# Kernel optimization log

Measured on AMD Instinct MI355X. Metric: run time of the kernel, lower is better.

Reference implementation:

```python
import jax, jax.numpy as jnp
import numpy as np

H = 32       # num_attention_heads
KV = 8       # num_key_value_heads
D = 128      # head_dim
HID = 4096   # hidden_size
EPS = 1e-6   # rms_norm_eps
BASE = 1000000.0  # rope_theta


def setup_inputs() -> dict:
    key = jax.random.key(0)
    ks = jax.random.split(key, 5)
    B, S = 1, 2048
    s = 0.02
    return {
        "x": jax.random.normal(ks[0], (B, S, HID), jnp.float32),
        "wq": jax.random.normal(ks[1], (H * D, HID), jnp.float32) * s,
        "wk": jax.random.normal(ks[2], (KV * D, HID), jnp.float32) * s,
        "wv": jax.random.normal(ks[3], (KV * D, HID), jnp.float32) * s,
        "wo": jax.random.normal(ks[4], (HID, H * D), jnp.float32) * s,
        "q_norm_w": jnp.ones((D,), jnp.float32),
        "k_norm_w": jnp.ones((D,), jnp.float32),
    }


def _rms(x, w):
    # F.rms_norm over last dim (head_dim), computed in fp32 then cast back
    x32 = x.astype(jnp.float32)
    y = x32 * jax.lax.rsqrt(jnp.mean(x32 * x32, axis=-1, keepdims=True) + EPS)
    return (y * w.astype(jnp.float32)).astype(x.dtype)


def _rope_tables(S, dtype):
    pair = jnp.arange(0, D, 2, dtype=jnp.float32)
    theta = 1.0 / (BASE ** (pair / D))                       # [D/2]
    ang = jnp.arange(S, dtype=jnp.float32)[:, None] * theta  # [S, D/2]
    ang = jnp.concatenate([ang, ang], axis=-1)               # [S, D]
    return jnp.cos(ang).astype(dtype), jnp.sin(ang).astype(dtype)


def _rope(x, cos, sin):
    # x: [B, H, S, D]; rotate_half convention (cat of two halves)
    half = D // 2
    rot = jnp.concatenate([-x[..., half:], x[..., :half]], axis=-1)
    return x * cos + rot * sin


def reference(x, wq, wk, wv, wo, q_norm_w, k_norm_w):
    B, S, _ = x.shape
    q = (x @ wq.T).reshape(B, S, H, D)
    k = (x @ wk.T).reshape(B, S, KV, D)
    v = (x @ wv.T).reshape(B, S, KV, D)
    q = _rms(q, q_norm_w).transpose(0, 2, 1, 3)   # [B, H, S, D]
    k = _rms(k, k_norm_w).transpose(0, 2, 1, 3)   # [B, KV, S, D]
    v = v.transpose(0, 2, 1, 3)                   # [B, KV, S, D]
    cos, sin = _rope_tables(S, x.dtype)
    q = _rope(q, cos, sin)
    k = _rope(k, cos, sin)
    # GQA: group Q heads over KV heads, causal SDPA
    G = H // KV
    qg = q.reshape(B, KV, G, S, D)
    scale = 1.0 / np.sqrt(D).astype(np.float32)
    scores = jnp.einsum('bkgsd,bktd->bkgst', qg, k) * scale  # [B,KV,G,S,S]
    causal = jnp.tril(jnp.ones((S, S), dtype=bool))
    scores = jnp.where(causal, scores, jnp.asarray(-jnp.inf, scores.dtype))
    p = jax.nn.softmax(scores, axis=-1)
    out = jnp.einsum('bkgst,bktd->bkgsd', p, v)               # [B,KV,G,S,D]
    out = out.reshape(B, H, S, D).transpose(0, 2, 1, 3).reshape(B, S, H * D)
    return out @ wo.T
```

## Files before the change

kernel.cpp:

```cpp
#include <hip/hip_runtime.h>
#include <hip/hip_bf16.h>

#define S_LEN   2048
#define HID_SZ  4096
#define NH      32
#define NKV     8
#define HD      128
#define EPS_F   1e-6f
#define SM_SCALE 0.08838834764831845f

typedef __attribute__((ext_vector_type(8))) short bf16x8;
typedef __attribute__((ext_vector_type(4))) float f32x4;

#define AS1(p) ((__attribute__((address_space(1))) void*)(p))
#define AS3(p) ((__attribute__((address_space(3))) void*)(p))

__device__ __forceinline__ short f2b(float f) {
  unsigned u = __builtin_bit_cast(unsigned, f);
  unsigned r = (u + 0x7fffu + ((u >> 16) & 1u)) >> 16;
  return (short)(unsigned short)r;
}

__global__ __launch_bounds__(256) void cvt_f32_bf16(const float* __restrict__ in,
                                                    short* __restrict__ out, int n4) {
  int i = blockIdx.x * 256 + threadIdx.x;
  if (i >= n4) return;
  float4 f = reinterpret_cast<const float4*>(in)[i];
  short4 o;
  o.x = f2b(f.x); o.y = f2b(f.y); o.z = f2b(f.z); o.w = f2b(f.w);
  reinterpret_cast<short4*>(out)[i] = o;
}

__global__ void rope_tables_k(float* __restrict__ cosT, float* __restrict__ sinT) {
  int s = blockIdx.x;
  int j = threadIdx.x;
  float theta = exp2f(-(float)(2 * j) * (19.931568569324174f / 128.0f));
  float ang = (float)s * theta;
  float sv, cv;
  sincosf(ang, &sv, &cv);
  cosT[s * 64 + j] = cv;
  sinT[s * 64 + j] = sv;
}

__global__ __launch_bounds__(256)
void rmsrope_k(const float* __restrict__ src, int srcStride, int srcCol,
               const float* __restrict__ w,
               const float* __restrict__ cosT, const float* __restrict__ sinT,
               short* __restrict__ dst, int heads) {
  int gw   = blockIdx.x * 4 + (threadIdx.x >> 6);
  int lane = threadIdx.x & 63;
  int s = gw / heads;
  int h = gw - s * heads;
  const float* p = src + (size_t)s * srcStride + srcCol + h * HD;
  float x0 = p[lane], x1 = p[lane + 64];
  float ss = x0 * x0 + x1 * x1;
#pragma unroll
  for (int off = 1; off < 64; off <<= 1) ss += __shfl_xor(ss, off);
  float r = rsqrtf(ss * (1.0f / 128.0f) + EPS_F);
  float y0 = x0 * r * w[lane];
  float y1 = x1 * r * w[lane + 64];
  float c = cosT[s * 64 + lane], sn = sinT[s * 64 + lane];
  float o0 = y0 * c - y1 * sn;
  float o1 = y1 * c + y0 * sn;
  short* d = dst + ((size_t)h * S_LEN + s) * HD;
  d[lane]      = f2b(o0);
  d[lane + 64] = f2b(o1);
}

__global__ __launch_bounds__(256)
void vtrans_k(const float* __restrict__ qkv, short* __restrict__ vt) {
  __shared__ float t[64][65];
  int s0 = blockIdx.x * 64;
  int d0 = blockIdx.y * 64;
  int kv = blockIdx.z;
  int j  = threadIdx.x & 63;
  int i0 = threadIdx.x >> 6;
#pragma unroll
  for (int r = 0; r < 16; ++r) {
    int i = i0 * 16 + r;
    t[i][j] = qkv[(size_t)(s0 + i) * 6144 + 5120 + kv * HD + d0 + j];
  }
  __syncthreads();
#pragma unroll
  for (int r = 0; r < 16; ++r) {
    int i = i0 * 16 + r;
    vt[((size_t)kv * HD + d0 + i) * S_LEN + s0 + j] = f2b(t[j][i]);
  }
}

__global__ __launch_bounds__(256)
void gemm_bt_k(const short* __restrict__ A, const short* __restrict__ B,
               float* __restrict__ C, int M, int N, int K) {
  __shared__ short As[128 * 32];
  __shared__ short Bs[128 * 32];
  int tid  = threadIdx.x;
  int lane = tid & 63;
  int wave = tid >> 6;
  int wr = wave >> 1, wc = wave & 1;
  int m0 = blockIdx.y * 128, n0 = blockIdx.x * 128;
  f32x4 acc[4][4] = {};
  int row16 = lane & 15;
  int kg    = (lane >> 4) << 3;
  int c0 = tid, c1 = tid + 256;
  const size_t rA0 = (size_t)(m0 + (c0 >> 2)) * K + ((c0 & 3) << 3);
  const size_t rA1 = (size_t)(m0 + (c1 >> 2)) * K + ((c1 & 3) << 3);
  const size_t rB0 = (size_t)(n0 + (c0 >> 2)) * K + ((c0 & 3) << 3);
  const size_t rB1 = (size_t)(n0 + (c1 >> 2)) * K + ((c1 & 3) << 3);
  for (int kt = 0; kt < K; kt += 32) {
    __builtin_amdgcn_global_load_lds(AS1(A + rA0 + kt), AS3(&As[c0 * 8]), 16, 0, 0);
    __builtin_amdgcn_global_load_lds(AS1(A + rA1 + kt), AS3(&As[c1 * 8]), 16, 0, 0);
    __builtin_amdgcn_global_load_lds(AS1(B + rB0 + kt), AS3(&Bs[c0 * 8]), 16, 0, 0);
    __builtin_amdgcn_global_load_lds(AS1(B + rB1 + kt), AS3(&Bs[c1 * 8]), 16, 0, 0);
    __syncthreads();
    bf16x8 af[4], bf[4];
#pragma unroll
    for (int i = 0; i < 4; ++i)
      af[i] = *reinterpret_cast<const bf16x8*>(&As[(wr * 64 + i * 16 + row16) * 32 + kg]);
#pragma unroll
    for (int j = 0; j < 4; ++j)
      bf[j] = *reinterpret_cast<const bf16x8*>(&Bs[(wc * 64 + j * 16 + row16) * 32 + kg]);
#pragma unroll
    for (int i = 0; i < 4; ++i)
#pragma unroll
      for (int j = 0; j < 4; ++j)
        acc[i][j] = __builtin_amdgcn_mfma_f32_16x16x32_bf16(af[i], bf[j], acc[i][j], 0, 0, 0);
    __syncthreads();
  }
  int rsub = (lane >> 4) << 2;
#pragma unroll
  for (int i = 0; i < 4; ++i)
#pragma unroll
    for (int j = 0; j < 4; ++j) {
      size_t base = (size_t)(m0 + wr * 64 + i * 16 + rsub) * N + (n0 + wc * 64 + j * 16 + row16);
#pragma unroll
      for (int reg = 0; reg < 4; ++reg)
        C[base + (size_t)reg * N] = acc[i][j][reg];
    }
}

__global__ __launch_bounds__(256)
void attn_k(const short* __restrict__ Qr, const short* __restrict__ Kr,
            const short* __restrict__ Vt, short* __restrict__ Ob) {
  constexpr int PP = 72;
  __shared__ short Kl[64 * 128];
  __shared__ short Vl[128 * 64];
  __shared__ short Pl[4][16 * PP];
  int qb = (int)gridDim.x - 1 - (int)blockIdx.x;
  int h  = blockIdx.y;
  int kvh = h >> 2;
  int tid = threadIdx.x, wave = tid >> 6, lane = tid & 63;
  int row16 = lane & 15, kg = (lane >> 4) << 3, rsub = (lane >> 4) << 2;
  int colb  = (lane >> 4) << 4;
  int swz   = (row16 & 7) << 4;
  int qrow0 = qb * 64 + wave * 16;

  bf16x8 qf[4];
  {
    const short* qp = Qr + ((size_t)h * S_LEN + qrow0 + row16) * HD + kg;
#pragma unroll
    for (int ks = 0; ks < 4; ++ks)
      qf[ks] = *reinterpret_cast<const bf16x8*>(qp + ks * 32);
  }
  f32x4 o[8] = {};
  float mrow[4], lrow[4];
#pragma unroll
  for (int r = 0; r < 4; ++r) { mrow[r] = -3.0e38f; lrow[r] = 0.0f; }

  const short* Kb = Kr + (size_t)kvh * S_LEN * HD;
  const short* Vb = Vt + (size_t)kvh * HD * S_LEN;

  for (int kt = 0; kt <= qb; ++kt) {
    const short* Kt = Kb + (size_t)kt * 64 * HD;
#pragma unroll
    for (int r = 0; r < 4; ++r) {
      int c = tid + r * 256;
      int krow = c >> 4, ch = c & 15;
      int sch = (ch & 8) | ((ch ^ krow) & 7);
      __builtin_amdgcn_global_load_lds(AS1(Kt + krow * HD + sch * 8),
                                       AS3(&Kl[c * 8]), 16, 0, 0);
    }
#pragma unroll
    for (int r = 0; r < 4; ++r) {
      int c = tid + r * 256;
      int dr = c >> 3, ch = c & 7;
      int sch = (ch ^ dr) & 7;
      __builtin_amdgcn_global_load_lds(AS1(Vb + (size_t)dr * S_LEN + kt * 64 + sch * 8),
                                       AS3(&Vl[c * 8]), 16, 0, 0);
    }
    __syncthreads();

    f32x4 s4[4];
#pragma unroll
    for (int nc = 0; nc < 4; ++nc) {
      int R = nc * 16 + row16;
      const char* rowp = (const char*)Kl + R * 256;
      f32x4 a = {};
#pragma unroll
      for (int ks = 0; ks < 4; ++ks) {
        bf16x8 kf = *reinterpret_cast<const bf16x8*>(rowp + ((ks * 64 + colb) ^ swz));
        a = __builtin_amdgcn_mfma_f32_16x16x32_bf16(qf[ks], kf, a, 0, 0, 0);
      }
      s4[nc] = a;
    }

    bool diag = (kt == qb);
    float mt[4] = {-3.0e38f, -3.0e38f, -3.0e38f, -3.0e38f};
#pragma unroll
    for (int nc = 0; nc < 4; ++nc)
#pragma unroll
      for (int reg = 0; reg < 4; ++reg) {
        float v = s4[nc][reg] * SM_SCALE;
        if (diag && (kt * 64 + nc * 16 + row16) > (qrow0 + rsub + reg)) v = -3.0e38f;
        s4[nc][reg] = v;
        mt[reg] = fmaxf(mt[reg], v);
      }
#pragma unroll
    for (int reg = 0; reg < 4; ++reg)
#pragma unroll
      for (int off = 1; off < 16; off <<= 1)
        mt[reg] = fmaxf(mt[reg], __shfl_xor(mt[reg], off));

    float sc[4], st[4];
#pragma unroll
    for (int reg = 0; reg < 4; ++reg) {
      float mnew = fmaxf(mrow[reg], mt[reg]);
      sc[reg] = __expf(mrow[reg] - mnew);
      mrow[reg] = mnew;
      st[reg] = 0.0f;
    }
#pragma unroll
    for (int nc = 0; nc < 4; ++nc)
#pragma unroll
      for (int reg = 0; reg < 4; ++reg) {
        float p = __expf(s4[nc][reg] - mrow[reg]);
        s4[nc][reg] = p;
        st[reg] += p;
      }
#pragma unroll
    for (int reg = 0; reg < 4; ++reg) {
#pragma unroll
      for (int off = 1; off < 16; off <<= 1)
        st[reg] += __shfl_xor(st[reg], off);
      lrow[reg] = lrow[reg] * sc[reg] + st[reg];
    }
#pragma unroll
    for (int i = 0; i < 8; ++i) {
      f32x4 t = o[i];
      t[0] *= sc[0]; t[1] *= sc[1]; t[2] *= sc[2]; t[3] *= sc[3];
      o[i] = t;
    }

#pragma unroll
    for (int nc = 0; nc < 4; ++nc)
#pragma unroll
      for (int reg = 0; reg < 4; ++reg)
        Pl[wave][(rsub + reg) * PP + nc * 16 + row16] = f2b(s4[nc][reg]);

#pragma unroll
    for (int ks = 0; ks < 2; ++ks) {
      bf16x8 pf = *reinterpret_cast<const bf16x8*>(&Pl[wave][row16 * PP + ks * 32 + kg]);
#pragma unroll
      for (int nc = 0; nc < 8; ++nc) {
        int R = nc * 16 + row16;
        const char* rowp = (const char*)Vl + R * 128;
        bf16x8 vf = *reinterpret_cast<const bf16x8*>(rowp + ((ks * 64 + colb) ^ swz));
        o[nc] = __builtin_amdgcn_mfma_f32_16x16x32_bf16(pf, vf, o[nc], 0, 0, 0);
      }
    }
    __syncthreads();
  }

#pragma unroll
  for (int nc = 0; nc < 8; ++nc)
#pragma unroll
    for (int reg = 0; reg < 4; ++reg) {
      float val = o[nc][reg] * (1.0f / lrow[reg]);
      int srow = qrow0 + rsub + reg;
      Ob[(size_t)srow * HID_SZ + h * HD + nc * 16 + row16] = f2b(val);
    }
}

extern "C" void kernel_launch(void* const* d_in, const int* in_sizes, int n_in,
                              void* d_out, int out_size, void* d_ws, size_t ws_size,
                              hipStream_t stream) {
  const float* x   = (const float*)d_in[0];
  const float* wq  = (const float*)d_in[1];
  const float* wk  = (const float*)d_in[2];
  const float* wv  = (const float*)d_in[3];
  const float* wo  = (const float*)d_in[4];
  const float* qnw = (const float*)d_in[5];
  const float* knw = (const float*)d_in[6];
  float* out = (float*)d_out;

  char* ws = (char*)d_ws;
  short* xb    = (short*)(ws);
  short* attnb = (short*)(ws);
  short* wqkvb = (short*)(ws + (16ull  << 20));
  short* wob   = (short*)(ws + (16ull  << 20));
  float* qkvf  = (float*)(ws + (64ull  << 20));
  short* qr    = (short*)(ws + (112ull << 20));
  short* kr    = (short*)(ws + (128ull << 20));
  short* vt    = (short*)(ws + (132ull << 20));
  float* cosT  = (float*)(ws + (136ull << 20));
  float* sinT  = (float*)(ws + (136ull << 20) + (512ull << 10));

  cvt_f32_bf16<<<8192,  256, 0, stream>>>(x,  xb,    2097152);
  cvt_f32_bf16<<<16384, 256, 0, stream>>>(wq, wqkvb,                       4194304);
  cvt_f32_bf16<<<4096,  256, 0, stream>>>(wk, wqkvb + (size_t)4096 * 4096, 1048576);
  cvt_f32_bf16<<<4096,  256, 0, stream>>>(wv, wqkvb + (size_t)5120 * 4096, 1048576);

  rope_tables_k<<<2048, 64, 0, stream>>>(cosT, sinT);

  gemm_bt_k<<<dim3(48, 16), 256, 0, stream>>>(xb, wqkvb, qkvf, 2048, 6144, 4096);

  cvt_f32_bf16<<<16384, 256, 0, stream>>>(wo, wob, 4194304);

  rmsrope_k<<<16384, 256, 0, stream>>>(qkvf, 6144, 0,    qnw, cosT, sinT, qr, NH);
  rmsrope_k<<<4096,  256, 0, stream>>>(qkvf, 6144, 4096, knw, cosT, sinT, kr, NKV);
  vtrans_k<<<dim3(32, 2, 8), 256, 0, stream>>>(qkvf, vt);

  attn_k<<<dim3(32, 32), 256, 0, stream>>>(qr, kr, vt, attnb);

  gemm_bt_k<<<dim3(32, 16), 256, 0, stream>>>(attnb, wob, out, 2048, 4096, 4096);

  (void)in_sizes; (void)n_in; (void)out_size; (void)ws_size;
}
```

Measured before the change: 637.8 us.

## Double-buffer attention K/V tiles, pair causal blocks, emit bf16 QKV, fold scale into Q

```diff
diff --git a/kernel.cpp b/kernel.cpp
--- a/kernel.cpp
+++ b/kernel.cpp
@@ -7,7 +7,7 @@
 #define NKV     8
 #define HD      128
 #define EPS_F   1e-6f
-#define SM_SCALE 0.08838834764831845f
+#define QSCALE  0.1275174475f
 
 typedef __attribute__((ext_vector_type(8))) short bf16x8;
 typedef __attribute__((ext_vector_type(4))) float f32x4;
@@ -19,6 +19,9 @@
   unsigned u = __builtin_bit_cast(unsigned, f);
   unsigned r = (u + 0x7fffu + ((u >> 16) & 1u)) >> 16;
   return (short)(unsigned short)r;
+}
+__device__ __forceinline__ float b2f(short s) {
+  return __builtin_bit_cast(float, (unsigned)((unsigned short)s) << 16);
 }
 
 __global__ __launch_bounds__(256) void cvt_f32_bf16(const float* __restrict__ in,
@@ -43,16 +46,16 @@
 }
 
 __global__ __launch_bounds__(256)
-void rmsrope_k(const float* __restrict__ src, int srcStride, int srcCol,
+void rmsrope_k(const short* __restrict__ src, int srcCol,
                const float* __restrict__ w,
                const float* __restrict__ cosT, const float* __restrict__ sinT,
-               short* __restrict__ dst, int heads) {
+               short* __restrict__ dst, int heads, float outScale) {
   int gw   = blockIdx.x * 4 + (threadIdx.x >> 6);
   int lane = threadIdx.x & 63;
   int s = gw / heads;
   int h = gw - s * heads;
-  const float* p = src + (size_t)s * srcStride + srcCol + h * HD;
-  float x0 = p[lane], x1 = p[lane + 64];
+  const short* p = src + (size_t)s * 6144 + srcCol + h * HD;
+  float x0 = b2f(p[lane]), x1 = b2f(p[lane + 64]);
   float ss = x0 * x0 + x1 * x1;
 #pragma unroll
   for (int off = 1; off < 64; off <<= 1) ss += __shfl_xor(ss, off);
@@ -60,16 +63,16 @@
   float y0 = x0 * r * w[lane];
   float y1 = x1 * r * w[lane + 64];
   float c = cosT[s * 64 + lane], sn = sinT[s * 64 + lane];
-  float o0 = y0 * c - y1 * sn;
-  float o1 = y1 * c + y0 * sn;
+  float o0 = (y0 * c - y1 * sn) * outScale;
+  float o1 = (y1 * c + y0 * sn) * outScale;
   short* d = dst + ((size_t)h * S_LEN + s) * HD;
   d[lane]      = f2b(o0);
   d[lane + 64] = f2b(o1);
 }
 
 __global__ __launch_bounds__(256)
-void vtrans_k(const float* __restrict__ qkv, short* __restrict__ vt) {
-  __shared__ float t[64][65];
+void vtrans_k(const short* __restrict__ qkvb, short* __restrict__ vt) {
+  __shared__ short t[64][65];
   int s0 = blockIdx.x * 64;
   int d0 = blockIdx.y * 64;
   int kv = blockIdx.z;
@@ -78,19 +81,20 @@
 #pragma unroll
   for (int r = 0; r < 16; ++r) {
     int i = i0 * 16 + r;
-    t[i][j] = qkv[(size_t)(s0 + i) * 6144 + 5120 + kv * HD + d0 + j];
+    t[i][j] = qkvb[(size_t)(s0 + i) * 6144 + 5120 + kv * HD + d0 + j];
   }
   __syncthreads();
 #pragma unroll
   for (int r = 0; r < 16; ++r) {
     int i = i0 * 16 + r;
-    vt[((size_t)kv * HD + d0 + i) * S_LEN + s0 + j] = f2b(t[j][i]);
-  }
-}
-
+    vt[((size_t)kv * HD + d0 + i) * S_LEN + s0 + j] = t[j][i];
+  }
+}
+
+template<bool BF16OUT>
 __global__ __launch_bounds__(256)
 void gemm_bt_k(const short* __restrict__ A, const short* __restrict__ B,
-               float* __restrict__ C, int M, int N, int K) {
+               void* __restrict__ Cv, int M, int N, int K) {
   __shared__ short As[128 * 32];
   __shared__ short Bs[128 * 32];
   int tid  = threadIdx.x;
@@ -133,8 +137,10 @@
     for (int j = 0; j < 4; ++j) {
       size_t base = (size_t)(m0 + wr * 64 + i * 16 + rsub) * N + (n0 + wc * 64 + j * 16 + row16);
 #pragma unroll
-      for (int reg = 0; reg < 4; ++reg)
-        C[base + (size_t)reg * N] = acc[i][j][reg];
+      for (int reg = 0; reg < 4; ++reg) {
+        if constexpr (BF16OUT) ((short*)Cv)[base + (size_t)reg * N] = f2b(acc[i][j][reg]);
+        else                   ((float*)Cv)[base + (size_t)reg * N] = acc[i][j][reg];
+      }
     }
 }
 
@@ -142,142 +148,164 @@
 void attn_k(const short* __restrict__ Qr, const short* __restrict__ Kr,
             const short* __restrict__ Vt, short* __restrict__ Ob) {
   constexpr int PP = 72;
-  __shared__ short Kl[64 * 128];
-  __shared__ short Vl[128 * 64];
+  __shared__ short Kl[2][64 * 128];
+  __shared__ short Vl[2][128 * 64];
   __shared__ short Pl[4][16 * PP];
-  int qb = (int)gridDim.x - 1 - (int)blockIdx.x;
-  int h  = blockIdx.y;
+  int pr  = blockIdx.x;
+  int h   = blockIdx.y;
   int kvh = h >> 2;
   int tid = threadIdx.x, wave = tid >> 6, lane = tid & 63;
   int row16 = lane & 15, kg = (lane >> 4) << 3, rsub = (lane >> 4) << 2;
   int colb  = (lane >> 4) << 4;
   int swz   = (row16 & 7) << 4;
-  int qrow0 = qb * 64 + wave * 16;
-
-  bf16x8 qf[4];
-  {
-    const short* qp = Qr + ((size_t)h * S_LEN + qrow0 + row16) * HD + kg;
-#pragma unroll
-    for (int ks = 0; ks < 4; ++ks)
-      qf[ks] = *reinterpret_cast<const bf16x8*>(qp + ks * 32);
-  }
-  f32x4 o[8] = {};
-  float mrow[4], lrow[4];
-#pragma unroll
-  for (int r = 0; r < 4; ++r) { mrow[r] = -3.0e38f; lrow[r] = 0.0f; }
 
   const short* Kb = Kr + (size_t)kvh * S_LEN * HD;
   const short* Vb = Vt + (size_t)kvh * HD * S_LEN;
 
-  for (int kt = 0; kt <= qb; ++kt) {
-    const short* Kt = Kb + (size_t)kt * 64 * HD;
-#pragma unroll
-    for (int r = 0; r < 4; ++r) {
-      int c = tid + r * 256;
-      int krow = c >> 4, ch = c & 15;
-      int sch = (ch & 8) | ((ch ^ krow) & 7);
-      __builtin_amdgcn_global_load_lds(AS1(Kt + krow * HD + sch * 8),
-                                       AS3(&Kl[c * 8]), 16, 0, 0);
+  int kso[4], vso[4], llo[4];
+#pragma unroll
+  for (int r = 0; r < 4; ++r) {
+    int c = tid + r * 256;
+    llo[r] = c * 8;
+    int krow = c >> 4, ch = c & 15;
+    int sch = (ch & 8) | ((ch ^ krow) & 7);
+    kso[r] = krow * HD + sch * 8;
+    int dr = c >> 3, vch = c & 7;
+    int vsch = (vch ^ dr) & 7;
+    vso[r] = dr * S_LEN + vsch * 8;
+  }
+
+#define STAGE(BUF, KT) do {                                                      \
+    const short* Kt_ = Kb + (size_t)(KT) * 64 * HD;                              \
+    const short* Vt_ = Vb + (KT) * 64;                                           \
+    _Pragma("unroll")                                                            \
+    for (int r_ = 0; r_ < 4; ++r_)                                               \
+      __builtin_amdgcn_global_load_lds(AS1(Kt_ + kso[r_]),                       \
+                                       AS3(&Kl[BUF][llo[r_]]), 16, 0, 0);        \
+    _Pragma("unroll")                                                            \
+    for (int r_ = 0; r_ < 4; ++r_)                                               \
+      __builtin_amdgcn_global_load_lds(AS1(Vt_ + vso[r_]),                       \
+                                       AS3(&Vl[BUF][llo[r_]]), 16, 0, 0);        \
+  } while (0)
+
+  STAGE(0, 0);
+
+  for (int half = 0; half < 2; ++half) {
+    int qb = half ? pr : (31 - pr);
+    int qrow0 = qb * 64 + wave * 16;
+
+    bf16x8 qf[4];
+    {
+      const short* qp = Qr + ((size_t)h * S_LEN + qrow0 + row16) * HD + kg;
+#pragma unroll
+      for (int ks = 0; ks < 4; ++ks)
+        qf[ks] = *reinterpret_cast<const bf16x8*>(qp + ks * 32);
     }
-#pragma unroll
-    for (int r = 0; r < 4; ++r) {
-      int c = tid + r * 256;
-      int dr = c >> 3, ch = c & 7;
-      int sch = (ch ^ dr) & 7;
-      __builtin_amdgcn_global_load_lds(AS1(Vb + (size_t)dr * S_LEN + kt * 64 + sch * 8),
-                                       AS3(&Vl[c * 8]), 16, 0, 0);
+    f32x4 o[8] = {};
+    float mrow[4], lrow[4];
+#pragma unroll
+    for (int r = 0; r < 4; ++r) { mrow[r] = -3.0e38f; lrow[r] = 0.0f; }
+
+    for (int kt = 0; kt <= qb; ++kt) {
+      int cur = kt & 1;
+      __syncthreads();
+      if (kt < qb) STAGE(cur ^ 1, kt + 1);
+
+      f32x4 s4[4];
+      __builtin_amdgcn_s_setprio(1);
+#pragma unroll
+      for (int nc = 0; nc < 4; ++nc) {
+        const char* rowp = (const char*)&Kl[cur][0] + (nc * 16 + row16) * 256;
+        f32x4 a = {};
+#pragma unroll
+        for (int ks = 0; ks < 4; ++ks) {
+          bf16x8 kf = *reinterpret_cast<const bf16x8*>(rowp + ((ks * 64 + colb) ^ swz));
+          a = __builtin_amdgcn_mfma_f32_16x16x32_bf16(qf[ks], kf, a, 0, 0, 0);
+        }
+        s4[nc] = a;
+      }
+      __builtin_amdgcn_s_setprio(0);
+
+      bool diag = (kt == qb);
+      float mt[4] = {-3.0e38f, -3.0e38f, -3.0e38f, -3.0e38f};
+#pragma unroll
+      for (int nc = 0; nc < 4; ++nc)
+#pragma unroll
+        for (int reg = 0; reg < 4; ++reg) {
+          float v = s4[nc][reg];
+          if (diag && (kt * 64 + nc * 16 + row16) > (qrow0 + rsub + reg)) v = -3.0e38f;
+          s4[nc][reg] = v;
+          mt[reg] = fmaxf(mt[reg], v);
+        }
+#pragma unroll
+      for (int reg = 0; reg < 4; ++reg)
+#pragma unroll
+        for (int off = 1; off < 16; off <<= 1)
+          mt[reg] = fmaxf(mt[reg], __shfl_xor(mt[reg], off));
+
+      float sc[4], st[4];
+#pragma unroll
+      for (int reg = 0; reg < 4; ++reg) {
+        float mnew = fmaxf(mrow[reg], mt[reg]);
+        sc[reg] = exp2f(mrow[reg] - mnew);
+        mrow[reg] = mnew;
+        st[reg] = 0.0f;
+      }
+#pragma unroll
+      for (int nc = 0; nc < 4; ++nc)
+#pragma unroll
+        for (int reg = 0; reg < 4; ++reg) {
+          float p = exp2f(s4[nc][reg] - mrow[reg]);
+          s4[nc][reg] = p;
+          st[reg] += p;
+        }
+#pragma unroll
+      for (int reg = 0; reg < 4; ++reg) {
+#pragma unroll
+        for (int off = 1; off < 16; off <<= 1)
+          st[reg] += __shfl_xor(st[reg], off);
+        lrow[reg] = lrow[reg] * sc[reg] + st[reg];
+      }
+#pragma unroll
+      for (int i = 0; i < 8; ++i) {
+        f32x4 t = o[i];
+        t[0] *= sc[0]; t[1] *= sc[1]; t[2] *= sc[2]; t[3] *= sc[3];
+        o[i] = t;
+      }
+
+#pragma unroll
+      for (int nc = 0; nc < 4; ++nc)
+#pragma unroll
+        for (int reg = 0; reg < 4; ++reg)
+          Pl[wave][(rsub + reg) * PP + nc * 16 + row16] = f2b(s4[nc][reg]);
+
+      __builtin_amdgcn_s_setprio(1);
+#pragma unroll
+      for (int ks = 0; ks < 2; ++ks) {
+        bf16x8 pf = *reinterpret_cast<const bf16x8*>(&Pl[wave][row16 * PP + ks * 32 + kg]);
+#pragma unroll
+        for (int nc = 0; nc < 8; ++nc) {
+          const char* rowp = (const char*)&Vl[cur][0] + (nc * 16 + row16) * 128;
+          bf16x8 vf = *reinterpret_cast<const bf16x8*>(rowp + ((ks * 64 + colb) ^ swz));
+          o[nc] = __builtin_amdgcn_mfma_f32_16x16x32_bf16(pf, vf, o[nc], 0, 0, 0);
+        }
+      }
+      __builtin_amdgcn_s_setprio(0);
     }
+
     __syncthreads();
-
-    f32x4 s4[4];
-#pragma unroll
-    for (int nc = 0; nc < 4; ++nc) {
-      int R = nc * 16 + row16;
-      const char* rowp = (const char*)Kl + R * 256;
-      f32x4 a = {};
-#pragma unroll
-      for (int ks = 0; ks < 4; ++ks) {
-        bf16x8 kf = *reinterpret_cast<const bf16x8*>(rowp + ((ks * 64 + colb) ^ swz));
-        a = __builtin_amdgcn_mfma_f32_16x16x32_bf16(qf[ks], kf, a, 0, 0, 0);
-      }
-      s4[nc] = a;
-    }
-
-    bool diag = (kt == qb);
-    float mt[4] = {-3.0e38f, -3.0e38f, -3.0e38f, -3.0e38f};
-#pragma unroll
-    for (int nc = 0; nc < 4; ++nc)
+    if (half == 0) STAGE(0, 0);
+
+#pragma unroll
+    for (int nc = 0; nc < 8; ++nc)
 #pragma unroll
       for (int reg = 0; reg < 4; ++reg) {
-        float v = s4[nc][reg] * SM_SCALE;
-        if (diag && (kt * 64 + nc * 16 + row16) > (qrow0 + rsub + reg)) v = -3.0e38f;
-        s4[nc][reg] = v;
-        mt[reg] = fmaxf(mt[reg], v);
-      }
-#pragma unroll
-    for (int reg = 0; reg < 4; ++reg)
-#pragma unroll
-      for (int off = 1; off < 16; off <<= 1)
-        mt[reg] = fmaxf(mt[reg], __shfl_xor(mt[reg], off));
-
-    float sc[4], st[4];
-#pragma unroll
-    for (int reg = 0; reg < 4; ++reg) {
-      float mnew = fmaxf(mrow[reg], mt[reg]);
-      sc[reg] = __expf(mrow[reg] - mnew);
-      mrow[reg] = mnew;
-      st[reg] = 0.0f;
-    }
-#pragma unroll
-    for (int nc = 0; nc < 4; ++nc)
-#pragma unroll
-      for (int reg = 0; reg < 4; ++reg) {
-        float p = __expf(s4[nc][reg] - mrow[reg]);
-        s4[nc][reg] = p;
-        st[reg] += p;
-      }
-#pragma unroll
-    for (int reg = 0; reg < 4; ++reg) {
-#pragma unroll
-      for (int off = 1; off < 16; off <<= 1)
-        st[reg] += __shfl_xor(st[reg], off);
-      lrow[reg] = lrow[reg] * sc[reg] + st[reg];
-    }
-#pragma unroll
-    for (int i = 0; i < 8; ++i) {
-      f32x4 t = o[i];
-      t[0] *= sc[0]; t[1] *= sc[1]; t[2] *= sc[2]; t[3] *= sc[3];
-      o[i] = t;
-    }
-
-#pragma unroll
-    for (int nc = 0; nc < 4; ++nc)
-#pragma unroll
-      for (int reg = 0; reg < 4; ++reg)
-        Pl[wave][(rsub + reg) * PP + nc * 16 + row16] = f2b(s4[nc][reg]);
-
-#pragma unroll
-    for (int ks = 0; ks < 2; ++ks) {
-      bf16x8 pf = *reinterpret_cast<const bf16x8*>(&Pl[wave][row16 * PP + ks * 32 + kg]);
-#pragma unroll
-      for (int nc = 0; nc < 8; ++nc) {
-        int R = nc * 16 + row16;
-        const char* rowp = (const char*)Vl + R * 128;
-        bf16x8 vf = *reinterpret_cast<const bf16x8*>(rowp + ((ks * 64 + colb) ^ swz));
-        o[nc] = __builtin_amdgcn_mfma_f32_16x16x32_bf16(pf, vf, o[nc], 0, 0, 0);
-      }
-    }
-    __syncthreads();
-  }
-
-#pragma unroll
-  for (int nc = 0; nc < 8; ++nc)
-#pragma unroll
-    for (int reg = 0; reg < 4; ++reg) {
-      float val = o[nc][reg] * (1.0f / lrow[reg]);
-      int srow = qrow0 + rsub + reg;
-      Ob[(size_t)srow * HID_SZ + h * HD + nc * 16 + row16] = f2b(val);
-    }
+        float val = o[nc][reg] * (1.0f / lrow[reg]);
+        int srow = qrow0 + rsub + reg;
+        Ob[(size_t)srow * HID_SZ + h * HD + nc * 16 + row16] = f2b(val);
+      }
+  }
+#undef STAGE
 }
 
 extern "C" void kernel_launch(void* const* d_in, const int* in_sizes, int n_in,
@@ -297,12 +325,12 @@
   short* attnb = (short*)(ws);
   short* wqkvb = (short*)(ws + (16ull  << 20));
   short* wob   = (short*)(ws + (16ull  << 20));
-  float* qkvf  = (float*)(ws + (64ull  << 20));
-  short* qr    = (short*)(ws + (112ull << 20));
-  short* kr    = (short*)(ws + (128ull << 20));
-  short* vt    = (short*)(ws + (132ull << 20));
-  float* cosT  = (float*)(ws + (136ull << 20));
-  float* sinT  = (float*)(ws + (136ull << 20) + (512ull << 10));
+  short* qkvb  = (short*)(ws + (64ull  << 20));
+  short* qr    = (short*)(ws + (88ull  << 20));
+  short* kr    = (short*)(ws + (104ull << 20));
+  short* vt    = (short*)(ws + (108ull << 20));
+  float* cosT  = (float*)(ws + (112ull << 20));
+  float* sinT  = (float*)(ws + (112ull << 20) + (512ull << 10));
 
   cvt_f32_bf16<<<8192,  256, 0, stream>>>(x,  xb,    2097152);
   cvt_f32_bf16<<<16384, 256, 0, stream>>>(wq, wqkvb,                       4194304);
@@ -311,17 +339,17 @@
 
   rope_tables_k<<<2048, 64, 0, stream>>>(cosT, sinT);
 
-  gemm_bt_k<<<dim3(48, 16), 256, 0, stream>>>(xb, wqkvb, qkvf, 2048, 6144, 4096);
+  gemm_bt_k<true><<<dim3(48, 16), 256, 0, stream>>>(xb, wqkvb, qkvb, 2048, 6144, 4096);
 
   cvt_f32_bf16<<<16384, 256, 0, stream>>>(wo, wob, 4194304);
 
-  rmsrope_k<<<16384, 256, 0, stream>>>(qkvf, 6144, 0,    qnw, cosT, sinT, qr, NH);
-  rmsrope_k<<<4096,  256, 0, stream>>>(qkvf, 6144, 4096, knw, cosT, sinT, kr, NKV);
-  vtrans_k<<<dim3(32, 2, 8), 256, 0, stream>>>(qkvf, vt);
-
-  attn_k<<<dim3(32, 32), 256, 0, stream>>>(qr, kr, vt, attnb);
-
-  gemm_bt_k<<<dim3(32, 16), 256, 0, stream>>>(attnb, wob, out, 2048, 4096, 4096);
+  rmsrope_k<<<16384, 256, 0, stream>>>(qkvb, 0,    qnw, cosT, sinT, qr, NH,  QSCALE);
+  rmsrope_k<<<4096,  256, 0, stream>>>(qkvb, 4096, knw, cosT, sinT, kr, NKV, 1.0f);
+  vtrans_k<<<dim3(32, 2, 8), 256, 0, stream>>>(qkvb, vt);
+
+  attn_k<<<dim3(16, 32), 256, 0, stream>>>(qr, kr, vt, attnb);
+
+  gemm_bt_k<false><<<dim3(32, 16), 256, 0, stream>>>(attnb, wob, out, 2048, 4096, 4096);
 
   (void)in_sizes; (void)n_in; (void)out_size; (void)ws_size;
 }
```

Result: faster. 555.3 us (-12.9%).
